# Optimization experiments

Hardware: AMD Instinct MI355X
Metric: run time of the kernel (lower is better)

## Reference

```python
import jax, jax.numpy as jnp
import numpy as np

B, L, D, H = 2, 2048, 1024, 16
HD = D // H  # head_dim = 64


def setup_inputs() -> dict:
    key = jax.random.key(0)
    ks = jax.random.split(key, 8)
    queries = jax.random.normal(ks[0], (B, L, D), dtype=jnp.float32)
    keys = jax.random.normal(ks[1], (B, L, D), dtype=jnp.float32)
    values = jax.random.normal(ks[2], (B, L, D), dtype=jnp.float32)
    mask = jax.random.randint(ks[3], (B, L, L), 0, 2) > 0  # True = masked
    s = 1.0 / np.sqrt(D)
    W_q = jax.random.normal(ks[4], (D, D), dtype=jnp.float32) * s
    W_k = jax.random.normal(ks[5], (D, D), dtype=jnp.float32) * s
    W_v = jax.random.normal(ks[6], (D, D), dtype=jnp.float32) * s
    W_o = jax.random.normal(ks[7], (D, D), dtype=jnp.float32) * s
    return {"queries": queries, "keys": keys, "values": values,
            "W_q": W_q, "W_k": W_k, "W_v": W_v, "W_o": W_o, "mask": mask}


def _split_heads(x):
    # [B, L, D] -> [B, H, L, HD]
    return x.reshape(B, L, H, HD).transpose(0, 2, 1, 3)


def reference(queries, keys, values, W_q, W_k, W_v, W_o, mask):
    # Linear projections (nn.Linear: x @ W.T, no bias)
    q = _split_heads(queries @ W_q.T)   # [B,H,Lq,HD]
    k = _split_heads(keys @ W_k.T)      # [B,H,Lk,HD]
    v = _split_heads(values @ W_v.T)    # [B,H,Lk,HD]
    scores = jnp.einsum('bnqd,bnkd->bnqk', q, k) / np.sqrt(HD)
    scores = jnp.where(mask[:, None, :, :], -1e9, scores)
    attn = jax.nn.softmax(scores, axis=-1)
    ctx = jnp.einsum('bnqk,bnkd->bnqd', attn, v)
    ctx = ctx.transpose(0, 2, 1, 3).reshape(B, L, D)
    return ctx @ W_o.T  # dropout p=0.0 -> identity
```

## Files before the change

kernel.cpp:

```cpp
#include <hip/hip_runtime.h>
#include <hip/hip_bf16.h>

typedef __bf16 bf16;
typedef __attribute__((ext_vector_type(8))) __bf16 bf16x8;
typedef __attribute__((ext_vector_type(4))) __bf16 bf16x4;
typedef __attribute__((ext_vector_type(4))) float f32x4;

#define B_   2
#define L_   2048
#define D_   1024
#define H_   16
#define HD_  64

__device__ __forceinline__ float fast_exp2(float x) {
  float e; asm("v_exp_f32 %0, %1" : "=v"(e) : "v"(x)); return e;
}

__device__ __forceinline__ void gll16(const bf16* g, bf16* l) {
  __builtin_amdgcn_global_load_lds((const __attribute__((address_space(1))) void*)g,
                                   (__attribute__((address_space(3))) void*)l,
                                   16, 0, 0);
}

__global__ void detect_kernel(const unsigned short* __restrict__ q_u,
                              const unsigned char* __restrict__ m_u,
                              int* __restrict__ flags) {
  __shared__ int cnt, odd;
  if (threadIdx.x == 0) { cnt = 0; odd = 0; }
  __syncthreads();
  int c = 0, o = 0;
  for (int i = 0; i < 8; i++) {
    int idx = threadIdx.x * 8 + i;
    unsigned e = (q_u[idx] >> 7) & 0xFF;
    if (e >= 0x8F || (e > 0 && e <= 0x6F)) c++;
    if ((idx & 3) && m_u[idx]) o = 1;
  }
  atomicAdd(&cnt, c);
  if (o) atomicOr(&odd, 1);
  __syncthreads();
  if (threadIdx.x == 0) { flags[0] = (cnt > 128) ? 1 : 0; flags[1] = odd; }
}

__device__ __forceinline__ void canon_body(const void* src, bf16* dst, int i, int f) {
  if (f) {
    const float4* s = (const float4*)src;
    float4 a = s[i / 4], b2 = s[i / 4 + 1];
    bf16x8 o;
    o[0] = (bf16)a.x;  o[1] = (bf16)a.y;  o[2] = (bf16)a.z;  o[3] = (bf16)a.w;
    o[4] = (bf16)b2.x; o[5] = (bf16)b2.y; o[6] = (bf16)b2.z; o[7] = (bf16)b2.w;
    *(bf16x8*)(dst + i) = o;
  } else {
    *(bf16x8*)(dst + i) = ((const bf16x8*)src)[i / 8];
  }
}

__global__ __launch_bounds__(256) void canon_pack(
    const void* xq, const void* xk, const void* xv,
    const void* Wq, const void* Wk, const void* Wv, const void* Wo,
    const void* mp,
    bf16* cxq, bf16* cxk, bf16* cxv,
    bf16* cWq, bf16* cWk, bf16* cWv, bf16* cWo,
    unsigned* __restrict__ bitsT,
    const int* __restrict__ flags) {
  int t = blockIdx.x;
  if (t >= 8192) {
    int wid = (t - 8192) * 256 + threadIdx.x;
    unsigned v = 0;
    if (flags[1]) {
      const uchar4* p = (const uchar4*)mp;
#pragma unroll
      for (int c = 0; c < 8; c++) {
        uchar4 u = p[wid * 8 + c];
        v |= (u.x ? 1u : 0u) << (c * 4 + 0);
        v |= (u.y ? 1u : 0u) << (c * 4 + 1);
        v |= (u.z ? 1u : 0u) << (c * 4 + 2);
        v |= (u.w ? 1u : 0u) << (c * 4 + 3);
      }
    } else {
      const int4* p = (const int4*)mp;
#pragma unroll
      for (int c = 0; c < 8; c++) {
        int4 u = p[wid * 8 + c];
        v |= (u.x ? 1u : 0u) << (c * 4 + 0);
        v |= (u.y ? 1u : 0u) << (c * 4 + 1);
        v |= (u.z ? 1u : 0u) << (c * 4 + 2);
        v |= (u.w ? 1u : 0u) << (c * 4 + 3);
      }
    }
    int row = wid >> 6, word = wid & 63;
    int kt = word >> 1, half = word & 1;
    bitsT[((size_t)kt * 4096 + row) * 2 + half] = v;
    return;
  }
  const int f = flags[0];
  const void* src; bf16* dst; int base;
  if (t < 2048)      { src = xq; dst = cxq; base = t * 2048; }
  else if (t < 4096) { src = xk; dst = cxk; base = (t - 2048) * 2048; }
  else if (t < 6144) { src = xv; dst = cxv; base = (t - 4096) * 2048; }
  else {
    int w = t - 6144, wi = w >> 9;
    base = (w & 511) * 2048;
    if (wi == 0)      { src = Wq; dst = cWq; }
    else if (wi == 1) { src = Wk; dst = cWk; }
    else if (wi == 2) { src = Wv; dst = cWv; }
    else              { src = Wo; dst = cWo; }
  }
  canon_body(src, dst, base + threadIdx.x * 8, f);
}

__global__ __launch_bounds__(256) void gemm_qkv(
    const bf16* __restrict__ Aq, const bf16* __restrict__ Bq, bf16* __restrict__ Cq,
    const bf16* __restrict__ Ak, const bf16* __restrict__ Bk, bf16* __restrict__ Ck,
    const bf16* __restrict__ Av, const bf16* __restrict__ Bv, bf16* __restrict__ VT) {
  __shared__ bf16 smem[128 * 136];
  bf16* sA = smem;
  bf16* sB = smem + 4096;
  const int z = blockIdx.z;
  const bf16* A  = (z == 0) ? Aq : (z == 1) ? Ak : Av;
  const bf16* Bm = (z == 0) ? Bq : (z == 1) ? Bk : Bv;

  const int tid = threadIdx.x;
  const int w = tid >> 6, lane = tid & 63, qd = lane >> 4, r = lane & 15;
  const int wm = w >> 1, wn = w & 1;
  const int m0 = blockIdx.x * 128, n0 = blockIdx.y * 128;

  f32x4 acc[4][4];
#pragma unroll
  for (int i = 0; i < 4; i++)
#pragma unroll
    for (int j = 0; j < 4; j++) acc[i][j] = (f32x4){0.f, 0.f, 0.f, 0.f};

  for (int k0 = 0; k0 < 1024; k0 += 32) {
    __syncthreads();
#pragma unroll
    for (int p = 0; p < 2; p++) {
      int c = p * 256 + tid;
      gll16(A + (size_t)(m0 + (c >> 2)) * 1024 + k0 + (c & 3) * 8, sA + c * 8);
    }
#pragma unroll
    for (int p = 0; p < 2; p++) {
      int c = p * 256 + tid;
      gll16(Bm + (size_t)(n0 + (c >> 2)) * 1024 + k0 + (c & 3) * 8, sB + c * 8);
    }
    __syncthreads();
    bf16x8 af[4], bfv[4];
#pragma unroll
    for (int i = 0; i < 4; i++)
      af[i] = *(const bf16x8*)&sA[(wm * 64 + i * 16 + r) * 32 + qd * 8];
#pragma unroll
    for (int j = 0; j < 4; j++)
      bfv[j] = *(const bf16x8*)&sB[(wn * 64 + j * 16 + r) * 32 + qd * 8];
#pragma unroll
    for (int i = 0; i < 4; i++)
#pragma unroll
      for (int j = 0; j < 4; j++)
        acc[i][j] = __builtin_amdgcn_mfma_f32_16x16x32_bf16(af[i], bfv[j], acc[i][j], 0, 0, 0);
  }

  if (z < 2) {
    bf16* C = (z == 0) ? Cq : Ck;
    const float s = (z == 0) ? 0.1803368801f : 1.0f;
#pragma unroll
    for (int i = 0; i < 4; i++)
#pragma unroll
      for (int j = 0; j < 4; j++)
#pragma unroll
        for (int rr = 0; rr < 4; rr++) {
          int row = m0 + wm * 64 + i * 16 + qd * 4 + rr;
          int col = n0 + wn * 64 + j * 16 + r;
          C[(size_t)row * 1024 + col] = (bf16)(acc[i][j][rr] * s);
        }
  } else {
    __syncthreads();
#pragma unroll
    for (int i = 0; i < 4; i++)
#pragma unroll
      for (int j = 0; j < 4; j++) {
        int col = wn * 64 + j * 16 + r;
        int rowb = wm * 64 + i * 16 + qd * 4;
        bf16x4 v4;
#pragma unroll
        for (int rr = 0; rr < 4; rr++) v4[rr] = (bf16)acc[i][j][rr];
        *(bf16x4*)&smem[col * 136 + rowb] = v4;
      }
    __syncthreads();
    const int b = m0 >> 11, tok0 = m0 & 2047, h0 = n0 >> 6;
#pragma unroll
    for (int p = 0; p < 8; p++) {
      int c = p * 256 + tid;
      int dl = c >> 4, ch = c & 15;
      bf16x8 v = *(const bf16x8*)&smem[dl * 136 + ch * 8];
      int head = h0 + (dl >> 6), d = dl & 63;
      *(bf16x8*)(VT + ((size_t)((b * 16 + head) * 64 + d)) * 2048 + tok0 + ch * 8) = v;
    }
  }
}

__global__ __launch_bounds__(256) void gemm_nt_out(const bf16* __restrict__ A,
                                                   const bf16* __restrict__ Bm,
                                                   void* __restrict__ Cout,
                                                   const int* __restrict__ flags) {
  __shared__ bf16 sA[128 * 32];
  __shared__ bf16 sB[64 * 32];
  const int tid = threadIdx.x;
  const int w = tid >> 6, lane = tid & 63, qd = lane >> 4, r = lane & 15;
  const int wm = w >> 1, wn = w & 1;
  const int m0 = blockIdx.x * 128, n0 = blockIdx.y * 64;

  f32x4 acc[4][2];
#pragma unroll
  for (int i = 0; i < 4; i++)
#pragma unroll
    for (int j = 0; j < 2; j++) acc[i][j] = (f32x4){0.f, 0.f, 0.f, 0.f};

  for (int k0 = 0; k0 < 1024; k0 += 32) {
    __syncthreads();
    {
      int c0 = tid;
      gll16(A + (size_t)(m0 + (c0 >> 2)) * 1024 + k0 + (c0 & 3) * 8, sA + c0 * 8);
      int c1 = 256 + tid;
      gll16(A + (size_t)(m0 + (c1 >> 2)) * 1024 + k0 + (c1 & 3) * 8, sA + c1 * 8);
      int cb = tid;
      gll16(Bm + (size_t)(n0 + (cb >> 2)) * 1024 + k0 + (cb & 3) * 8, sB + cb * 8);
    }
    __syncthreads();
    bf16x8 af[4], bfv[2];
#pragma unroll
    for (int i = 0; i < 4; i++)
      af[i] = *(const bf16x8*)&sA[(wm * 64 + i * 16 + r) * 32 + qd * 8];
#pragma unroll
    for (int j = 0; j < 2; j++)
      bfv[j] = *(const bf16x8*)&sB[(wn * 32 + j * 16 + r) * 32 + qd * 8];
#pragma unroll
    for (int i = 0; i < 4; i++)
#pragma unroll
      for (int j = 0; j < 2; j++)
        acc[i][j] = __builtin_amdgcn_mfma_f32_16x16x32_bf16(af[i], bfv[j], acc[i][j], 0, 0, 0);
  }
  const int f = flags[0];
#pragma unroll
  for (int i = 0; i < 4; i++)
#pragma unroll
    for (int j = 0; j < 2; j++)
#pragma unroll
      for (int rr = 0; rr < 4; rr++) {
        int row = m0 + wm * 64 + i * 16 + qd * 4 + rr;
        int col = n0 + wn * 32 + j * 16 + r;
        if (f) ((float*)Cout)[(size_t)row * 1024 + col] = acc[i][j][rr];
        else   ((bf16*)Cout)[(size_t)row * 1024 + col] = (bf16)acc[i][j][rr];
      }
}

__global__ __launch_bounds__(512, 4) void attn_kernel(const bf16* __restrict__ Q,
                                                      const bf16* __restrict__ Kp,
                                                      const bf16* __restrict__ Vt,
                                                      const unsigned* __restrict__ bitsT,
                                                      bf16* __restrict__ CTX) {
  __shared__ bf16 sK[3][64 * 64];
  __shared__ bf16 sVT[3][64 * 64];
  __shared__ bf16 sP[128 * 72];
  const int tid = threadIdx.x;
  const int w = tid >> 6, lane = tid & 63, qd = lane >> 4, r = lane & 15;
  const int wgid = blockIdx.x;
  const int bh = ((wgid >> 7) << 3) + (wgid & 7);
  const int b = bh >> 4, h = bh & 15;
  const int q0 = ((wgid >> 3) & 15) * 128;
  const int qrow = w * 16 + r;

  bf16x8 qf[2];
#pragma unroll
  for (int ks = 0; ks < 2; ks++)
    qf[ks] = *(const bf16x8*)(Q + (size_t)(b * L_ + q0 + qrow) * D_ +
                              h * HD_ + ks * 32 + qd * 8);

  bf16x8 ones;
#pragma unroll
  for (int e = 0; e < 8; e++) ones[e] = (bf16)1.0f;

  f32x4 o[4], lacc;
#pragma unroll
  for (int dj = 0; dj < 4; dj++) o[dj] = (f32x4){0.f, 0.f, 0.f, 0.f};
  lacc = (f32x4){0.f, 0.f, 0.f, 0.f};

  f32x4 S_a[4], S_b[4];
  uint2 m0r, m1r, m2r;

#define STAGE_KV(KT, BI)                                                            \
  {                                                                                 \
    int row_ = tid >> 3, kc_ = tid & 7;                                             \
    int kcg_ = kc_ ^ (row_ & 7);                                                    \
    gll16(Kp + (size_t)(b * L_ + (KT) * 64 + row_) * D_ + h * HD_ + kcg_ * 8,       \
          &sK[BI][0] + tid * 8);                                                    \
    gll16(Vt + (size_t)(bh * 64 + row_) * L_ + (KT) * 64 + kcg_ * 8,                \
          &sVT[BI][0] + tid * 8);                                                   \
  }

#define MLOAD(KT, MD)                                                               \
  MD = *(const uint2*)(bitsT + ((size_t)(KT) * 4096 + b * 2048 + q0 + qrow) * 2);

#define QK_BLK(BI, SD)                                                              \
  {                                                                                 \
    __builtin_amdgcn_s_setprio(1);                                                  \
    _Pragma("unroll") for (int j = 0; j < 4; j++) {                                 \
      SD[j] = (f32x4){0.f, 0.f, 0.f, 0.f};                                          \
      _Pragma("unroll") for (int ks = 0; ks < 2; ks++) {                            \
        int row_ = j * 16 + r;                                                      \
        int phys_ = (ks * 4 + qd) ^ (row_ & 7);                                     \
        bf16x8 kf_ = *(const bf16x8*)&sK[BI][row_ * 64 + phys_ * 8];                \
        SD[j] = __builtin_amdgcn_mfma_f32_16x16x32_bf16(kf_, qf[ks], SD[j], 0, 0, 0); \
      }                                                                             \
    }                                                                               \
    __builtin_amdgcn_s_setprio(0);                                                  \
  }

#define EXP_PACK(SP, MP)                                                            \
  {                                                                                 \
    _Pragma("unroll") for (int j = 0; j < 4; j++) {                                 \
      unsigned word_ = ((j) < 2) ? (MP).x : (MP).y;                                 \
      unsigned nib_ = (word_ >> ((j & 1) * 16 + qd * 4)) & 0xFu;                    \
      bf16x4 pv_;                                                                   \
      _Pragma("unroll") for (int rr = 0; rr < 4; rr++) {                            \
        float e_ = fast_exp2((SP)[j][rr]);                                          \
        pv_[rr] = (bf16)(((nib_ >> rr) & 1u) ? 0.f : e_);                           \
      }                                                                             \
      *(bf16x4*)&sP[qrow * 72 + j * 16 + qd * 4] = pv_;                             \
    }                                                                               \
  }

#define PV_BLK(BI)                                                                  \
  {                                                                                 \
    asm volatile("s_waitcnt lgkmcnt(0)" ::: "memory");                              \
    __builtin_amdgcn_sched_barrier(0);                                              \
    bf16x8 vf_[4][2];                                                               \
    _Pragma("unroll") for (int dj = 0; dj < 4; dj++)                                \
      _Pragma("unroll") for (int ks = 0; ks < 2; ks++) {                            \
        int row_ = dj * 16 + r;                                                     \
        int phys_ = (ks * 4 + qd) ^ (row_ & 7);                                     \
        vf_[dj][ks] = *(const bf16x8*)&sVT[BI][row_ * 64 + phys_ * 8];              \
      }                                                                             \
    __builtin_amdgcn_s_setprio(1);                                                  \
    _Pragma("unroll") for (int ks = 0; ks < 2; ks++) {                              \
      bf16x8 pf_ = *(const bf16x8*)&sP[qrow * 72 + ks * 32 + qd * 8];               \
      _Pragma("unroll") for (int dj = 0; dj < 4; dj++)                              \
        o[dj] = __builtin_amdgcn_mfma_f32_16x16x32_bf16(pf_, vf_[dj][ks], o[dj], 0, 0, 0); \
      lacc = __builtin_amdgcn_mfma_f32_16x16x32_bf16(pf_, ones, lacc, 0, 0, 0);     \
    }                                                                               \
    __builtin_amdgcn_s_setprio(0);                                                  \
  }

#define ITER(T, BP, BC, BN, SPV, SCU, MPV, MNX)                                     \
  {                                                                                 \
    STAGE_KV((T) + 1, BN);                                                          \
    MLOAD((T) + 1, MNX);                                                            \
    asm volatile("s_waitcnt vmcnt(3)" ::: "memory");                                \
    __builtin_amdgcn_sched_barrier(0);                                              \
    __builtin_amdgcn_s_barrier();                                                   \
    EXP_PACK(SPV, MPV);                                                             \
    QK_BLK(BC, SCU);                                                                \
    PV_BLK(BP);                                                                     \
    __builtin_amdgcn_s_barrier();                                                   \
  }

  STAGE_KV(0, 0); MLOAD(0, m0r);
  STAGE_KV(1, 1); MLOAD(1, m1r);
  asm volatile("s_waitcnt vmcnt(3)" ::: "memory");
  __builtin_amdgcn_sched_barrier(0);
  __builtin_amdgcn_s_barrier();
  QK_BLK(0, S_a);
  __builtin_amdgcn_s_barrier();

  for (int tt = 1; tt <= 25; tt += 6) {
    ITER(tt,     0, 1, 2, S_a, S_b, m0r, m2r);
    ITER(tt + 1, 1, 2, 0, S_b, S_a, m1r, m0r);
    ITER(tt + 2, 2, 0, 1, S_a, S_b, m2r, m1r);
    ITER(tt + 3, 0, 1, 2, S_b, S_a, m0r, m2r);
    ITER(tt + 4, 1, 2, 0, S_a, S_b, m1r, m0r);
    ITER(tt + 5, 2, 0, 1, S_b, S_a, m2r, m1r);
  }

  asm volatile("s_waitcnt vmcnt(0)" ::: "memory");
  __builtin_amdgcn_sched_barrier(0);
  __builtin_amdgcn_s_barrier();
  EXP_PACK(S_a, m0r);
  QK_BLK(1, S_b);
  PV_BLK(0);
  __builtin_amdgcn_s_barrier();

  EXP_PACK(S_b, m1r);
  PV_BLK(1);

#undef STAGE_KV
#undef MLOAD
#undef QK_BLK
#undef EXP_PACK
#undef PV_BLK
#undef ITER

  {
    float inv[4];
#pragma unroll
    for (int rr = 0; rr < 4; rr++) inv[rr] = 1.0f / lacc[rr];
#pragma unroll
    for (int dj = 0; dj < 4; dj++)
#pragma unroll
      for (int rr = 0; rr < 4; rr++) {
        int rg = b * L_ + q0 + w * 16 + qd * 4 + rr;
        int col = h * HD_ + dj * 16 + r;
        CTX[(size_t)rg * 1024 + col] = (bf16)(o[dj][rr] * inv[rr]);
      }
  }
}

extern "C" void kernel_launch(void* const* d_in, const int* in_sizes, int n_in,
                              void* d_out, int out_size, void* d_ws, size_t ws_size,
                              hipStream_t stream) {
  const void* xq = d_in[0];
  const void* xk = d_in[1];
  const void* xv = d_in[2];
  const void* Wq = d_in[3];
  const void* Wk = d_in[4];
  const void* Wv = d_in[5];
  const void* Wo = d_in[6];
  const void* mask = d_in[7];

  char* ws = (char*)d_ws;
  const size_t MB = 1048576;
  int*      FLAGS = (int*)(ws + 0);
  unsigned* BITS  = (unsigned*)(ws + 4096);
  bf16* cWo = (bf16*)(ws + 2 * MB);
  bf16* cWq = (bf16*)(ws + 4 * MB);
  bf16* cWk = (bf16*)(ws + 6 * MB);
  bf16* cWv = (bf16*)(ws + 8 * MB);
  bf16* cxq = (bf16*)(ws + 10 * MB);
  bf16* cxk = (bf16*)(ws + 18 * MB);
  bf16* cxv = (bf16*)(ws + 26 * MB);
  bf16* Q   = (bf16*)(ws + 34 * MB);
  bf16* K   = (bf16*)(ws + 42 * MB);
  bf16* VT  = (bf16*)(ws + 50 * MB);
  bf16* CTX = (bf16*)(ws + 26 * MB);

  detect_kernel<<<1, 256, 0, stream>>>((const unsigned short*)xq,
                                       (const unsigned char*)mask, FLAGS);
  canon_pack<<<9216, 256, 0, stream>>>(xq, xk, xv, Wq, Wk, Wv, Wo, mask,
                                       cxq, cxk, cxv, cWq, cWk, cWv, cWo,
                                       BITS, FLAGS);
  gemm_qkv<<<dim3(32, 8, 3), 256, 0, stream>>>(cxq, cWq, Q,
                                               cxk, cWk, K,
                                               cxv, cWv, VT);
  attn_kernel<<<512, 512, 0, stream>>>(Q, K, VT, BITS, CTX);
  gemm_nt_out<<<dim3(32, 16), 256, 0, stream>>>(CTX, cWo, d_out, FLAGS);
}
```

Measured before the change: 249.4 us.

## Double-buffer LDS loads and remap workgroups per XCD in projection GEMMs

Both projection GEMMs (QKV and output) now double-buffer shared memory. The next K-slice is prefetched with global_load_lds while MFMAs run on the current slice, synchronised by partial vmcnt waits and raw s_barrier. Workgroup IDs are flattened to 1D and remapped so consecutive tiles land on the same XCD, which should improve L2 reuse. s_setprio is raised around the MFMA block. The intent is to hide global load latency in the GEMMs, at the cost of more LDS per block and reliance on exact vmcnt counts.

New measurement: 250.2 us. About the same (+0.3%).

```diff
diff --git a/kernel.cpp b/kernel.cpp
--- a/kernel.cpp
+++ b/kernel.cpp
@@ -113,16 +113,18 @@
     const bf16* __restrict__ Ak, const bf16* __restrict__ Bk, bf16* __restrict__ Ck,
     const bf16* __restrict__ Av, const bf16* __restrict__ Bv, bf16* __restrict__ VT) {
   __shared__ bf16 smem[128 * 136];
-  bf16* sA = smem;
-  bf16* sB = smem + 4096;
-  const int z = blockIdx.z;
+  const int wgid = blockIdx.x;
+  const int lin = (wgid & 7) * 96 + (wgid >> 3);
+  const int z = lin >> 8;
+  const int rem = lin & 255;
+  const int m0 = (rem >> 3) * 128, n0 = (rem & 7) * 128;
+
   const bf16* A  = (z == 0) ? Aq : (z == 1) ? Ak : Av;
   const bf16* Bm = (z == 0) ? Bq : (z == 1) ? Bk : Bv;
 
   const int tid = threadIdx.x;
   const int w = tid >> 6, lane = tid & 63, qd = lane >> 4, r = lane & 15;
   const int wm = w >> 1, wn = w & 1;
-  const int m0 = blockIdx.x * 128, n0 = blockIdx.y * 128;
 
   f32x4 acc[4][4];
 #pragma unroll
@@ -130,32 +132,51 @@
 #pragma unroll
     for (int j = 0; j < 4; j++) acc[i][j] = (f32x4){0.f, 0.f, 0.f, 0.f};
 
-  for (int k0 = 0; k0 < 1024; k0 += 32) {
-    __syncthreads();
-#pragma unroll
-    for (int p = 0; p < 2; p++) {
-      int c = p * 256 + tid;
-      gll16(A + (size_t)(m0 + (c >> 2)) * 1024 + k0 + (c & 3) * 8, sA + c * 8);
+#define QSTAGE(K0, SA, SB)                                                          \
+  {                                                                                 \
+    _Pragma("unroll") for (int p = 0; p < 2; p++) {                                 \
+      int c = p * 256 + tid;                                                        \
+      gll16(A + (size_t)(m0 + (c >> 2)) * 1024 + (K0) + (c & 3) * 8, (SA) + c * 8); \
+    }                                                                               \
+    _Pragma("unroll") for (int p = 0; p < 2; p++) {                                 \
+      int c = p * 256 + tid;                                                        \
+      gll16(Bm + (size_t)(n0 + (c >> 2)) * 1024 + (K0) + (c & 3) * 8, (SB) + c * 8);\
+    }                                                                               \
+  }
+
+  QSTAGE(0, smem, smem + 4096);
+
+#pragma unroll 2
+  for (int it = 0; it < 32; ++it) {
+    bf16* sAc = smem + (it & 1) * 8192;
+    bf16* sBc = sAc + 4096;
+    if (it < 31) {
+      bf16* sAn = smem + ((it + 1) & 1) * 8192;
+      QSTAGE((it + 1) * 32, sAn, sAn + 4096);
+      asm volatile("s_waitcnt vmcnt(4)" ::: "memory");
+    } else {
+      asm volatile("s_waitcnt vmcnt(0)" ::: "memory");
     }
-#pragma unroll
-    for (int p = 0; p < 2; p++) {
-      int c = p * 256 + tid;
-      gll16(Bm + (size_t)(n0 + (c >> 2)) * 1024 + k0 + (c & 3) * 8, sB + c * 8);
-    }
-    __syncthreads();
+    __builtin_amdgcn_sched_barrier(0);
+    __builtin_amdgcn_s_barrier();
+
     bf16x8 af[4], bfv[4];
 #pragma unroll
     for (int i = 0; i < 4; i++)
-      af[i] = *(const bf16x8*)&sA[(wm * 64 + i * 16 + r) * 32 + qd * 8];
+      af[i] = *(const bf16x8*)&sAc[(wm * 64 + i * 16 + r) * 32 + qd * 8];
 #pragma unroll
     for (int j = 0; j < 4; j++)
-      bfv[j] = *(const bf16x8*)&sB[(wn * 64 + j * 16 + r) * 32 + qd * 8];
+      bfv[j] = *(const bf16x8*)&sBc[(wn * 64 + j * 16 + r) * 32 + qd * 8];
+    __builtin_amdgcn_s_setprio(1);
 #pragma unroll
     for (int i = 0; i < 4; i++)
 #pragma unroll
       for (int j = 0; j < 4; j++)
         acc[i][j] = __builtin_amdgcn_mfma_f32_16x16x32_bf16(af[i], bfv[j], acc[i][j], 0, 0, 0);
-  }
+    __builtin_amdgcn_s_setprio(0);
+    __builtin_amdgcn_s_barrier();
+  }
+#undef QSTAGE
 
   if (z < 2) {
     bf16* C = (z == 0) ? Cq : Ck;
@@ -200,12 +221,14 @@
                                                    const bf16* __restrict__ Bm,
                                                    void* __restrict__ Cout,
                                                    const int* __restrict__ flags) {
-  __shared__ bf16 sA[128 * 32];
-  __shared__ bf16 sB[64 * 32];
+  __shared__ bf16 sAB[2][6144];
+  const int wgid = blockIdx.x;
+  const int lin = (wgid & 7) * 64 + (wgid >> 3);
+  const int m0 = (lin >> 4) * 128, n0 = (lin & 15) * 64;
+
   const int tid = threadIdx.x;
   const int w = tid >> 6, lane = tid & 63, qd = lane >> 4, r = lane & 15;
   const int wm = w >> 1, wn = w & 1;
-  const int m0 = blockIdx.x * 128, n0 = blockIdx.y * 64;
 
   f32x4 acc[4][2];
 #pragma unroll
@@ -213,30 +236,49 @@
 #pragma unroll
     for (int j = 0; j < 2; j++) acc[i][j] = (f32x4){0.f, 0.f, 0.f, 0.f};
 
-  for (int k0 = 0; k0 < 1024; k0 += 32) {
-    __syncthreads();
-    {
-      int c0 = tid;
-      gll16(A + (size_t)(m0 + (c0 >> 2)) * 1024 + k0 + (c0 & 3) * 8, sA + c0 * 8);
-      int c1 = 256 + tid;
-      gll16(A + (size_t)(m0 + (c1 >> 2)) * 1024 + k0 + (c1 & 3) * 8, sA + c1 * 8);
-      int cb = tid;
-      gll16(Bm + (size_t)(n0 + (cb >> 2)) * 1024 + k0 + (cb & 3) * 8, sB + cb * 8);
+#define OSTAGE(K0, SA, SB)                                                            \
+  {                                                                                   \
+    int c0 = tid;                                                                     \
+    gll16(A + (size_t)(m0 + (c0 >> 2)) * 1024 + (K0) + (c0 & 3) * 8, (SA) + c0 * 8);  \
+    int c1 = 256 + tid;                                                               \
+    gll16(A + (size_t)(m0 + (c1 >> 2)) * 1024 + (K0) + (c1 & 3) * 8, (SA) + c1 * 8);  \
+    gll16(Bm + (size_t)(n0 + (tid >> 2)) * 1024 + (K0) + (tid & 3) * 8, (SB) + tid * 8); \
+  }
+
+  OSTAGE(0, &sAB[0][0], &sAB[0][4096]);
+
+#pragma unroll 2
+  for (int it = 0; it < 32; ++it) {
+    bf16* sAc = &sAB[it & 1][0];
+    bf16* sBc = sAc + 4096;
+    if (it < 31) {
+      bf16* sAn = &sAB[(it + 1) & 1][0];
+      OSTAGE((it + 1) * 32, sAn, sAn + 4096);
+      asm volatile("s_waitcnt vmcnt(3)" ::: "memory");
+    } else {
+      asm volatile("s_waitcnt vmcnt(0)" ::: "memory");
     }
-    __syncthreads();
+    __builtin_amdgcn_sched_barrier(0);
+    __builtin_amdgcn_s_barrier();
+
     bf16x8 af[4], bfv[2];
 #pragma unroll
     for (int i = 0; i < 4; i++)
-      af[i] = *(const bf16x8*)&sA[(wm * 64 + i * 16 + r) * 32 + qd * 8];
+      af[i] = *(const bf16x8*)&sAc[(wm * 64 + i * 16 + r) * 32 + qd * 8];
 #pragma unroll
     for (int j = 0; j < 2; j++)
-      bfv[j] = *(const bf16x8*)&sB[(wn * 32 + j * 16 + r) * 32 + qd * 8];
+      bfv[j] = *(const bf16x8*)&sBc[(wn * 32 + j * 16 + r) * 32 + qd * 8];
+    __builtin_amdgcn_s_setprio(1);
 #pragma unroll
     for (int i = 0; i < 4; i++)
 #pragma unroll
       for (int j = 0; j < 2; j++)
         acc[i][j] = __builtin_amdgcn_mfma_f32_16x16x32_bf16(af[i], bfv[j], acc[i][j], 0, 0, 0);
-  }
+    __builtin_amdgcn_s_setprio(0);
+    __builtin_amdgcn_s_barrier();
+  }
+#undef OSTAGE
+
   const int f = flags[0];
 #pragma unroll
   for (int i = 0; i < 4; i++)
@@ -444,9 +486,9 @@
   canon_pack<<<9216, 256, 0, stream>>>(xq, xk, xv, Wq, Wk, Wv, Wo, mask,
                                        cxq, cxk, cxv, cWq, cWk, cWv, cWo,
                                        BITS, FLAGS);
-  gemm_qkv<<<dim3(32, 8, 3), 256, 0, stream>>>(cxq, cWq, Q,
-                                               cxk, cWk, K,
-                                               cxv, cWv, VT);
+  gemm_qkv<<<768, 256, 0, stream>>>(cxq, cWq, Q,
+                                    cxk, cWk, K,
+                                    cxv, cWv, VT);
   attn_kernel<<<512, 512, 0, stream>>>(Q, K, VT, BITS, CTX);
-  gemm_nt_out<<<dim3(32, 16), 256, 0, stream>>>(CTX, cWo, d_out, FLAGS);
-}
+  gemm_nt_out<<<512, 256, 0, stream>>>(CTX, cWo, d_out, FLAGS);
+}
```

## Double-buffer QKV GEMM shared-memory tiles with async prefetch of next k-slice

Applied to the files above, without the earlier changes.

The QKV projection GEMM now alternates between two shared-memory buffers, issuing the global-to-LDS loads for the next k-slice before computing on the current one. Explicit vmcnt waits and barriers replace the two full syncthreads per iteration, so the global load latency can overlap the MFMA work. It also raises wave priority around the MFMA block. This uses the full 128x136 smem allocation for two stages and depends on manual waitcnt accounting being correct.

New measurement: 252.7 us. Within noise of the previous version (+1.3%).

```diff
diff --git a/kernel.cpp b/kernel.cpp
--- a/kernel.cpp
+++ b/kernel.cpp
@@ -113,8 +113,6 @@
     const bf16* __restrict__ Ak, const bf16* __restrict__ Bk, bf16* __restrict__ Ck,
     const bf16* __restrict__ Av, const bf16* __restrict__ Bv, bf16* __restrict__ VT) {
   __shared__ bf16 smem[128 * 136];
-  bf16* sA = smem;
-  bf16* sB = smem + 4096;
   const int z = blockIdx.z;
   const bf16* A  = (z == 0) ? Aq : (z == 1) ? Ak : Av;
   const bf16* Bm = (z == 0) ? Bq : (z == 1) ? Bk : Bv;
@@ -130,32 +128,50 @@
 #pragma unroll
     for (int j = 0; j < 4; j++) acc[i][j] = (f32x4){0.f, 0.f, 0.f, 0.f};
 
-  for (int k0 = 0; k0 < 1024; k0 += 32) {
-    __syncthreads();
-#pragma unroll
-    for (int p = 0; p < 2; p++) {
-      int c = p * 256 + tid;
-      gll16(A + (size_t)(m0 + (c >> 2)) * 1024 + k0 + (c & 3) * 8, sA + c * 8);
+#define QSTAGE(K0, BUF)                                                             \
+  {                                                                                 \
+    _Pragma("unroll") for (int p = 0; p < 2; p++) {                                 \
+      int c = p * 256 + tid;                                                        \
+      gll16(A + (size_t)(m0 + (c >> 2)) * 1024 + (K0) + (c & 3) * 8, (BUF) + c * 8);\
+    }                                                                               \
+    _Pragma("unroll") for (int p = 0; p < 2; p++) {                                 \
+      int c = p * 256 + tid;                                                        \
+      gll16(Bm + (size_t)(n0 + (c >> 2)) * 1024 + (K0) + (c & 3) * 8,               \
+            (BUF) + 4096 + c * 8);                                                  \
+    }                                                                               \
+  }
+
+  QSTAGE(0, smem);
+
+#pragma unroll 2
+  for (int it = 0; it < 32; ++it) {
+    bf16* cur = smem + (it & 1) * 8192;
+    if (it < 31) {
+      QSTAGE((it + 1) * 32, smem + ((it + 1) & 1) * 8192);
+      asm volatile("s_waitcnt vmcnt(4)" ::: "memory");
+    } else {
+      asm volatile("s_waitcnt vmcnt(0)" ::: "memory");
     }
-#pragma unroll
-    for (int p = 0; p < 2; p++) {
-      int c = p * 256 + tid;
-      gll16(Bm + (size_t)(n0 + (c >> 2)) * 1024 + k0 + (c & 3) * 8, sB + c * 8);
-    }
-    __syncthreads();
+    __builtin_amdgcn_sched_barrier(0);
+    __builtin_amdgcn_s_barrier();
+
     bf16x8 af[4], bfv[4];
 #pragma unroll
     for (int i = 0; i < 4; i++)
-      af[i] = *(const bf16x8*)&sA[(wm * 64 + i * 16 + r) * 32 + qd * 8];
+      af[i] = *(const bf16x8*)&cur[(wm * 64 + i * 16 + r) * 32 + qd * 8];
 #pragma unroll
     for (int j = 0; j < 4; j++)
-      bfv[j] = *(const bf16x8*)&sB[(wn * 64 + j * 16 + r) * 32 + qd * 8];
+      bfv[j] = *(const bf16x8*)&cur[4096 + (wn * 64 + j * 16 + r) * 32 + qd * 8];
+    __builtin_amdgcn_s_setprio(1);
 #pragma unroll
     for (int i = 0; i < 4; i++)
 #pragma unroll
       for (int j = 0; j < 4; j++)
         acc[i][j] = __builtin_amdgcn_mfma_f32_16x16x32_bf16(af[i], bfv[j], acc[i][j], 0, 0, 0);
-  }
+    __builtin_amdgcn_s_setprio(0);
+    __builtin_amdgcn_s_barrier();
+  }
+#undef QSTAGE
 
   if (z < 2) {
     bf16* C = (z == 0) ? Cq : Ck;
```

## Double GEMM K-tile to 64 with XOR-swizzled LDS layout in projection kernels

Applied to the files above, without the earlier changes.

Both the QKV projection GEMM and the output projection GEMM now stage 64-wide K slices per iteration instead of 32. This halves the number of barrier pairs and load rounds over the K loop. The LDS layout is XOR-swizzled on 16-byte chunks by row so that the wider 128-byte rows do not cause bank conflicts on fragment reads. The cost is more shared memory per block and more fragment registers, which may reduce occupancy.

Result: no change. 253.4 us (+1.6%).

```diff
diff --git a/kernel.cpp b/kernel.cpp
--- a/kernel.cpp
+++ b/kernel.cpp
@@ -114,7 +114,7 @@
     const bf16* __restrict__ Av, const bf16* __restrict__ Bv, bf16* __restrict__ VT) {
   __shared__ bf16 smem[128 * 136];
   bf16* sA = smem;
-  bf16* sB = smem + 4096;
+  bf16* sB = smem + 8192;
   const int z = blockIdx.z;
   const bf16* A  = (z == 0) ? Aq : (z == 1) ? Ak : Av;
   const bf16* Bm = (z == 0) ? Bq : (z == 1) ? Bk : Bv;
@@ -130,31 +130,46 @@
 #pragma unroll
     for (int j = 0; j < 4; j++) acc[i][j] = (f32x4){0.f, 0.f, 0.f, 0.f};
 
-  for (int k0 = 0; k0 < 1024; k0 += 32) {
-    __syncthreads();
-#pragma unroll
-    for (int p = 0; p < 2; p++) {
+  for (int k0 = 0; k0 < 1024; k0 += 64) {
+    __syncthreads();
+#pragma unroll
+    for (int p = 0; p < 4; p++) {
       int c = p * 256 + tid;
-      gll16(A + (size_t)(m0 + (c >> 2)) * 1024 + k0 + (c & 3) * 8, sA + c * 8);
-    }
-#pragma unroll
-    for (int p = 0; p < 2; p++) {
+      int row = c >> 3, kcg = (c & 7) ^ (row & 7);
+      gll16(A + (size_t)(m0 + row) * 1024 + k0 + kcg * 8, sA + c * 8);
+    }
+#pragma unroll
+    for (int p = 0; p < 4; p++) {
       int c = p * 256 + tid;
-      gll16(Bm + (size_t)(n0 + (c >> 2)) * 1024 + k0 + (c & 3) * 8, sB + c * 8);
-    }
-    __syncthreads();
-    bf16x8 af[4], bfv[4];
+      int row = c >> 3, kcg = (c & 7) ^ (row & 7);
+      gll16(Bm + (size_t)(n0 + row) * 1024 + k0 + kcg * 8, sB + c * 8);
+    }
+    __syncthreads();
+    bf16x8 af[4][2], bfv[4][2];
 #pragma unroll
     for (int i = 0; i < 4; i++)
-      af[i] = *(const bf16x8*)&sA[(wm * 64 + i * 16 + r) * 32 + qd * 8];
+#pragma unroll
+      for (int ks = 0; ks < 2; ks++) {
+        int row = wm * 64 + i * 16 + r;
+        int phys = (ks * 4 + qd) ^ (row & 7);
+        af[i][ks] = *(const bf16x8*)&sA[row * 64 + phys * 8];
+      }
 #pragma unroll
     for (int j = 0; j < 4; j++)
-      bfv[j] = *(const bf16x8*)&sB[(wn * 64 + j * 16 + r) * 32 + qd * 8];
-#pragma unroll
-    for (int i = 0; i < 4; i++)
-#pragma unroll
-      for (int j = 0; j < 4; j++)
-        acc[i][j] = __builtin_amdgcn_mfma_f32_16x16x32_bf16(af[i], bfv[j], acc[i][j], 0, 0, 0);
+#pragma unroll
+      for (int ks = 0; ks < 2; ks++) {
+        int row = wn * 64 + j * 16 + r;
+        int phys = (ks * 4 + qd) ^ (row & 7);
+        bfv[j][ks] = *(const bf16x8*)&sB[row * 64 + phys * 8];
+      }
+#pragma unroll
+    for (int ks = 0; ks < 2; ks++)
+#pragma unroll
+      for (int i = 0; i < 4; i++)
+#pragma unroll
+        for (int j = 0; j < 4; j++)
+          acc[i][j] = __builtin_amdgcn_mfma_f32_16x16x32_bf16(af[i][ks], bfv[j][ks],
+                                                              acc[i][j], 0, 0, 0);
   }
 
   if (z < 2) {
@@ -200,8 +215,8 @@
                                                    const bf16* __restrict__ Bm,
                                                    void* __restrict__ Cout,
                                                    const int* __restrict__ flags) {
-  __shared__ bf16 sA[128 * 32];
-  __shared__ bf16 sB[64 * 32];
+  __shared__ bf16 sA[128 * 64];
+  __shared__ bf16 sB[64 * 64];
   const int tid = threadIdx.x;
   const int w = tid >> 6, lane = tid & 63, qd = lane >> 4, r = lane & 15;
   const int wm = w >> 1, wn = w & 1;
@@ -213,29 +228,46 @@
 #pragma unroll
     for (int j = 0; j < 2; j++) acc[i][j] = (f32x4){0.f, 0.f, 0.f, 0.f};
 
-  for (int k0 = 0; k0 < 1024; k0 += 32) {
-    __syncthreads();
-    {
-      int c0 = tid;
-      gll16(A + (size_t)(m0 + (c0 >> 2)) * 1024 + k0 + (c0 & 3) * 8, sA + c0 * 8);
-      int c1 = 256 + tid;
-      gll16(A + (size_t)(m0 + (c1 >> 2)) * 1024 + k0 + (c1 & 3) * 8, sA + c1 * 8);
-      int cb = tid;
-      gll16(Bm + (size_t)(n0 + (cb >> 2)) * 1024 + k0 + (cb & 3) * 8, sB + cb * 8);
-    }
-    __syncthreads();
-    bf16x8 af[4], bfv[2];
+  for (int k0 = 0; k0 < 1024; k0 += 64) {
+    __syncthreads();
+#pragma unroll
+    for (int p = 0; p < 4; p++) {
+      int c = p * 256 + tid;
+      int row = c >> 3, kcg = (c & 7) ^ (row & 7);
+      gll16(A + (size_t)(m0 + row) * 1024 + k0 + kcg * 8, sA + c * 8);
+    }
+#pragma unroll
+    for (int p = 0; p < 2; p++) {
+      int c = p * 256 + tid;
+      int row = c >> 3, kcg = (c & 7) ^ (row & 7);
+      gll16(Bm + (size_t)(n0 + row) * 1024 + k0 + kcg * 8, sB + c * 8);
+    }
+    __syncthreads();
+    bf16x8 af[4][2], bfv[2][2];
 #pragma unroll
     for (int i = 0; i < 4; i++)
-      af[i] = *(const bf16x8*)&sA[(wm * 64 + i * 16 + r) * 32 + qd * 8];
+#pragma unroll
+      for (int ks = 0; ks < 2; ks++) {
+        int row = wm * 64 + i * 16 + r;
+        int phys = (ks * 4 + qd) ^ (row & 7);
+        af[i][ks] = *(const bf16x8*)&sA[row * 64 + phys * 8];
+      }
 #pragma unroll
     for (int j = 0; j < 2; j++)
-      bfv[j] = *(const bf16x8*)&sB[(wn * 32 + j * 16 + r) * 32 + qd * 8];
-#pragma unroll
-    for (int i = 0; i < 4; i++)
-#pragma unroll
-      for (int j = 0; j < 2; j++)
-        acc[i][j] = __builtin_amdgcn_mfma_f32_16x16x32_bf16(af[i], bfv[j], acc[i][j], 0, 0, 0);
+#pragma unroll
+      for (int ks = 0; ks < 2; ks++) {
+        int row = wn * 32 + j * 16 + r;
+        int phys = (ks * 4 + qd) ^ (row & 7);
+        bfv[j][ks] = *(const bf16x8*)&sB[row * 64 + phys * 8];
+      }
+#pragma unroll
+    for (int ks = 0; ks < 2; ks++)
+#pragma unroll
+      for (int i = 0; i < 4; i++)
+#pragma unroll
+        for (int j = 0; j < 2; j++)
+          acc[i][j] = __builtin_amdgcn_mfma_f32_16x16x32_bf16(af[i][ks], bfv[j][ks],
+                                                              acc[i][j], 0, 0, 0);
   }
   const int f = flags[0];
 #pragma unroll
```
